# Performance work log

Measured on AMD Instinct MI355X. Metric: run time of the kernel, lower is better.

## Reference

```python
import jax, jax.numpy as jnp
import numpy as np

N = 50000
E = 800000
IN_DIM = 128
HIDDEN = 256
HP = HIDDEN // 3            # 85
HP2 = HIDDEN - 2 * HP       # 86
OUT_DIM = 40


def setup_inputs() -> dict:
    key = jax.random.key(0)
    ks = jax.random.split(key, 10)
    x = jax.random.normal(ks[0], (N, IN_DIM), dtype=jnp.float32)
    edge_index = jax.random.randint(ks[1], (2, E), 0, N, dtype=jnp.int64)
    s = 1.0 / np.sqrt(IN_DIM)
    W0 = jax.random.uniform(ks[2], (IN_DIM, HP), jnp.float32, -s, s)
    b0 = jax.random.uniform(ks[3], (HP,), jnp.float32, -s, s)
    W1 = jax.random.uniform(ks[4], (IN_DIM, HP), jnp.float32, -s, s)
    b1 = jax.random.uniform(ks[5], (HP,), jnp.float32, -s, s)
    W2 = jax.random.uniform(ks[6], (IN_DIM, HP2), jnp.float32, -s, s)
    b2 = jax.random.uniform(ks[7], (HP2,), jnp.float32, -s, s)
    sf = 1.0 / np.sqrt(HIDDEN)
    Wf = jax.random.uniform(ks[8], (HIDDEN, OUT_DIM), jnp.float32, -sf, sf)
    bf = jax.random.uniform(ks[9], (OUT_DIM,), jnp.float32, -sf, sf)
    return {"x": x, "edge_index": edge_index, "W0": W0, "b0": b0,
            "W1": W1, "b1": b1, "W2": W2, "b2": b2, "Wf": Wf, "bf": bf}


def _spmm(row, col, x, n):
    # adj @ x where adj[row[e], col[e]] = 1 : gather neighbor feats, scatter-add to row
    return jax.ops.segment_sum(x[col], row, num_segments=n)


def reference(x, edge_index, W0, b0, W1, b1, W2, b2, Wf, bf):
    n = x.shape[0]
    row, col = edge_index[0], edge_index[1]
    # out-degree of row nodes, clamped to min 1
    deg = jax.ops.segment_sum(jnp.ones((row.shape[0],), x.dtype), row, num_segments=n)
    deg_inv = 1.0 / jnp.maximum(deg, 1.0)
    # hop 0
    h0 = x @ W0 + b0
    # hop 1: (A x) * deg_inv
    ax = _spmm(row, col, x, n)
    h1 = (ax * deg_inv[:, None]) @ W1 + b1
    # hop 2: (A A x) * deg_inv^2
    aax = _spmm(row, col, ax, n)
    h2 = (aax * (deg_inv ** 2)[:, None]) @ W2 + b2
    h = jax.nn.relu(jnp.concatenate([h0, h1, h2], axis=1))
    # dropout inactive in eval mode
    return h @ Wf + bf
```

## Files before the change

kernel.cpp:

```cpp
#include <hip/hip_runtime.h>

#define N_NODES 50000
#define E_EDGES 800000
#define IN_DIM  128
#define OUT_DIM 40
#define NPAD    50176
#define NBKT    196
#define NBLK    256
#define EPB     3125

#define OFF_CNT   0
#define OFF_BASE  50176
#define OFF_DEG   100352
#define OFF_RS    150528
#define OFF_EPACK 200704
#define OFF_SCOL  1000704
#define OFF_WTBF  1800704
#define OFF_WF2T  1819136
#define OFF_BV    1826048
#define OFF_XBF   1826336
#define OFF_AXBF  (OFF_XBF  + NPAD * 64)
#define OFF_AAXBF (OFF_AXBF + NPAD * 64)
#define OFF_BTOT  (OFF_AAXBF + NPAD * 64)
#define OFF_BOFF  (OFF_BTOT + 256)

typedef short bf16x8 __attribute__((ext_vector_type(8)));
typedef float f32x4  __attribute__((ext_vector_type(4)));

__device__ __forceinline__ short f2bf(float f) {
    unsigned u = __float_as_uint(f);
    unsigned r = u + 0x7FFFu + ((u >> 16) & 1u);
    return (short)(r >> 16);
}

__device__ __forceinline__ bf16x8 cvt8(float4 a, float4 b) {
    bf16x8 v;
    v[0] = f2bf(a.x); v[1] = f2bf(a.y); v[2] = f2bf(a.z); v[3] = f2bf(a.w);
    v[4] = f2bf(b.x); v[5] = f2bf(b.y); v[6] = f2bf(b.z); v[7] = f2bf(b.w);
    return v;
}

__device__ __forceinline__ int block_excl_scan_256(int v, int* total_out,
                                                   int* wtot )
{
    const int t = threadIdx.x;
    const int lane = t & 63, wid = t >> 6;
    int sc = v;
    #pragma unroll
    for (int off = 1; off < 64; off <<= 1) {
        int tmp = __shfl_up(sc, off, 64);
        if (lane >= off) sc += tmp;
    }
    if (lane == 63) wtot[wid] = sc;
    __syncthreads();
    if (t == 0) {
        int a = 0;
        #pragma unroll
        for (int w2 = 0; w2 < 4; ++w2) { int tmp = wtot[w2]; wtot[w2] = a; a += tmp; }
        wtot[4] = a;
    }
    __syncthreads();
    *total_out = wtot[4];
    return sc - v + wtot[wid];
}

__global__ __launch_bounds__(256) void prep_kernel(
    const float* __restrict__ x, short* __restrict__ xbf,
    const int* __restrict__ row, int* __restrict__ cnt,
    const float* __restrict__ W0, const float* __restrict__ b0,
    const float* __restrict__ W1, const float* __restrict__ b1,
    const float* __restrict__ W2, const float* __restrict__ b2,
    const float* __restrict__ Wf,
    short* __restrict__ Wtbf, short* __restrict__ Wf2t,
    float* __restrict__ biasv)
{
    __shared__ int lbin[NBKT];
    const int t = threadIdx.x;
    const int b = blockIdx.x;

    if (b < 3136) {
        int idx = b * 256 + t;
        int node = idx >> 4;
        bf16x8 v;
        if (node < N_NODES) {
            const float4* rp = (const float4*)x + (size_t)idx * 2;
            v = cvt8(rp[0], rp[1]);
        } else {
            #pragma unroll
            for (int j = 0; j < 8; ++j) v[j] = 0;
        }
        *(bf16x8*)(xbf + (size_t)idx * 8) = v;
    } else if (b < 3136 + NBLK) {
        const int blk = b - 3136;
        if (t < NBKT) lbin[t] = 0;
        __syncthreads();
        const int e0 = blk * EPB;
        for (int i = t; i < EPB; i += 256)
            atomicAdd(&lbin[row[e0 + i] >> 8], 1);
        __syncthreads();
        if (t < NBKT) cnt[t * NBLK + blk] = lbin[t];
    } else {
        int idx = (b - 3392) * 256 + t;
        if (idx < 288 * 128) {
            int v = idx >> 7, k = idx & 127;
            int s = v / 96, local = v - 96 * s;
            float val = 0.0f;
            if (s == 0 && local < 85)      val = W0[k * 85 + local];
            else if (s == 1 && local < 85) val = W1[k * 85 + local];
            else if (s == 2 && local < 86) val = W2[k * 86 + local];
            Wtbf[idx] = f2bf(val);
        } else if (idx < 288 * 128 + 48 * 288) {
            int j2 = idx - 288 * 128;
            int c = j2 / 288, v = j2 - c * 288;
            int s = v / 96, local = v - 96 * s;
            float val = 0.0f;
            if (c < OUT_DIM && local < ((s == 2) ? 86 : 85))
                val = Wf[(s * 85 + local) * OUT_DIM + c];
            Wf2t[j2] = f2bf(val);
        } else if (idx < 288 * 128 + 48 * 288 + 288) {
            int v = idx - (288 * 128 + 48 * 288);
            int s = v / 96, local = v - 96 * s;
            float val = 0.0f;
            if (s == 0 && local < 85)      val = b0[local];
            else if (s == 1 && local < 85) val = b1[local];
            else if (s == 2 && local < 86) val = b2[local];
            biasv[v] = val;
        }
    }
}

__global__ __launch_bounds__(256) void scan_local_kernel(
    const int* __restrict__ cnt, int* __restrict__ base,
    int* __restrict__ btot)
{
    __shared__ int wtot[5];
    const int b = blockIdx.x;
    const int t = threadIdx.x;
    int v = cnt[b * NBLK + t];
    int total;
    int excl = block_excl_scan_256(v, &total, wtot);
    base[b * NBLK + t] = excl;
    if (t == 0) btot[b] = total;
}

__global__ __launch_bounds__(256) void scan_add_kernel(
    const int* __restrict__ btot, int* __restrict__ base)
{
    __shared__ int wtot[5];
    __shared__ int sh[256];
    const int t = threadIdx.x;
    const int b = blockIdx.x;
    int v = (t < NBKT) ? btot[t] : 0;
    int total;
    int excl = block_excl_scan_256(v, &total, wtot);
    sh[t] = excl;
    __syncthreads();
    int off = sh[b];
    base[b * NBLK + t] += off;
}

__global__ __launch_bounds__(256) void scatter_coarse_kernel(
    const int* __restrict__ row, const int* __restrict__ col,
    const int* __restrict__ base, unsigned int* __restrict__ epack)
{
    __shared__ int lcnt[NBKT];
    __shared__ int lbs[NBKT];
    const int t   = threadIdx.x;
    const int blk = blockIdx.x;
    if (t < NBKT) { lcnt[t] = 0; lbs[t] = base[t * NBLK + blk]; }
    __syncthreads();
    const int e0 = blk * EPB;
    for (int i = t; i < EPB; i += 256) {
        int r = row[e0 + i];
        int c = col[e0 + i];
        int cb = r >> 8;
        int loc = atomicAdd(&lcnt[cb], 1);
        epack[lbs[cb] + loc] = ((unsigned)(r & 255) << 16) | (unsigned)c;
    }
}

__global__ __launch_bounds__(256) void fine_sort_kernel(
    const unsigned int* __restrict__ epack,
    const int* __restrict__ base,
    int* __restrict__ sorted_col,
    int* __restrict__ deg, int* __restrict__ row_start)
{
    __shared__ int lhist[256];
    __shared__ int lbase[256];
    __shared__ int wtot[5];
    const int t  = threadIdx.x;
    const int cb = blockIdx.x;
    const int s  = base[cb * NBLK];
    const int e2 = (cb == NBKT - 1) ? E_EDGES : base[(cb + 1) * NBLK];

    lhist[t] = 0;
    __syncthreads();
    for (int i = s + t; i < e2; i += 256)
        atomicAdd(&lhist[epack[i] >> 16], 1);
    __syncthreads();

    int v = lhist[t];
    int total;
    int excl = block_excl_scan_256(v, &total, wtot);

    int node = cb * 256 + t;
    deg[node]       = v;
    row_start[node] = s + excl;
    lbase[t] = excl;
    __syncthreads();
    lhist[t] = 0;
    __syncthreads();

    for (int i = s + t; i < e2; i += 256) {
        unsigned p = epack[i];
        int rlo = p >> 16;
        int off = atomicAdd(&lhist[rlo], 1);
        sorted_col[s + lbase[rlo] + off] = (int)(p & 0xFFFFu);
    }
}

__global__ __launch_bounds__(256) void spmm_gather_kernel(
    const short* __restrict__ src,
    const int*   __restrict__ row_start,
    const int*   __restrict__ sorted_col,
    short*       __restrict__ dst)
{
    int node = (blockIdx.x * 256 + threadIdx.x) >> 4;
    int lane = threadIdx.x & 15;
    if (node >= N_NODES) return;
    int s = row_start[node];
    int e = row_start[node + 1];

    float acc[8];
    #pragma unroll
    for (int j = 0; j < 8; ++j) acc[j] = 0.0f;

    for (int i = s; i < e; i += 8) {
        const int nn = e - i;
        int cidx[8];
        #pragma unroll
        for (int j = 0; j < 8; ++j)
            cidx[j] = sorted_col[i + (j < nn ? j : 0)];
        uint4 v[8];
        #pragma unroll
        for (int j = 0; j < 8; ++j)
            v[j] = *(const uint4*)(src + (size_t)cidx[j] * IN_DIM + lane * 8);
        #pragma unroll
        for (int j = 0; j < 8; ++j) {
            if (j < nn) {
                acc[0] += __uint_as_float(v[j].x << 16);
                acc[1] += __uint_as_float(v[j].x & 0xFFFF0000u);
                acc[2] += __uint_as_float(v[j].y << 16);
                acc[3] += __uint_as_float(v[j].y & 0xFFFF0000u);
                acc[4] += __uint_as_float(v[j].z << 16);
                acc[5] += __uint_as_float(v[j].z & 0xFFFF0000u);
                acc[6] += __uint_as_float(v[j].w << 16);
                acc[7] += __uint_as_float(v[j].w & 0xFFFF0000u);
            }
        }
    }
    bf16x8 r;
    #pragma unroll
    for (int j = 0; j < 8; ++j) r[j] = f2bf(acc[j]);
    *(bf16x8*)(dst + (size_t)node * IN_DIM + lane * 8) = r;
}

#define HTS 296

__global__ __launch_bounds__(256) void dense_fused_kernel(
    const short* __restrict__ xbf,
    const short* __restrict__ axbf,
    const short* __restrict__ aaxbf,
    const int*   __restrict__ deg,
    const short* __restrict__ Wtbf,
    const short* __restrict__ Wf2t,
    const float* __restrict__ biasv,
    const float* __restrict__ bfin,
    float* __restrict__ out)
{
    __shared__ short wbuf[96 * 132];
    __shared__ short htile[64 * HTS];

    const int tid  = threadIdx.x;
    const int w    = tid >> 6;
    const int lane = tid & 63;
    const int il   = lane & 15;
    const int kq   = lane >> 4;
    const int m0   = blockIdx.x * 64 + w * 16;

    float dvj[4];
    #pragma unroll
    for (int j = 0; j < 4; ++j) {
        int node = m0 + kq * 4 + j;
        dvj[j] = 1.0f / fmaxf((float)deg[node], 1.0f);
    }

    #pragma unroll
    for (int s = 0; s < 3; ++s) {
        #pragma unroll
        for (int j = 0; j < 6; ++j) {
            int idx  = tid + j * 256;
            int brow = idx >> 4;
            int slot = idx & 15;
            uint4 v = *(const uint4*)(Wtbf + (size_t)(s * 96 + brow) * IN_DIM + slot * 8);
            *(uint4*)(wbuf + brow * 132 + slot * 8) = v;
        }
        __syncthreads();

        const short* __restrict__ src = (s == 0) ? xbf : (s == 1) ? axbf : aaxbf;
        const int arow = m0 + il;

        f32x4 acc[6];
        #pragma unroll
        for (int c = 0; c < 6; ++c)
            #pragma unroll
            for (int q = 0; q < 4; ++q) acc[c][q] = 0.0f;

        #pragma unroll
        for (int kk = 0; kk < 4; ++kk) {
            bf16x8 afrag = *(const bf16x8*)(
                src + (size_t)arow * IN_DIM + kk * 32 + kq * 8);
            #pragma unroll
            for (int c = 0; c < 6; ++c) {
                bf16x8 bfrag = *(const bf16x8*)(
                    wbuf + (c * 16 + il) * 132 + kk * 32 + kq * 8);
                acc[c] = __builtin_amdgcn_mfma_f32_16x16x32_bf16(
                    afrag, bfrag, acc[c], 0, 0, 0);
            }
        }

        #pragma unroll
        for (int j = 0; j < 4; ++j) {
            int nl = w * 16 + kq * 4 + j;
            float sc = (s == 0) ? 1.0f : (s == 1) ? dvj[j] : dvj[j] * dvj[j];
            #pragma unroll
            for (int c = 0; c < 6; ++c) {
                int vcol = s * 96 + c * 16 + il;
                float hv = fmaf(acc[c][j], sc, biasv[vcol]);
                htile[nl * HTS + vcol] = f2bf(fmaxf(hv, 0.0f));
            }
        }
        __syncthreads();
    }

    f32x4 acc2[3];
    #pragma unroll
    for (int cc = 0; cc < 3; ++cc)
        #pragma unroll
        for (int q = 0; q < 4; ++q) acc2[cc][q] = 0.0f;

    #pragma unroll
    for (int kk = 0; kk < 9; ++kk) {
        bf16x8 afrag = *(const bf16x8*)(
            htile + (w * 16 + il) * HTS + kk * 32 + kq * 8);
        #pragma unroll
        for (int cc = 0; cc < 3; ++cc) {
            bf16x8 bfrag = *(const bf16x8*)(
                Wf2t + (size_t)(cc * 16 + il) * 288 + kk * 32 + kq * 8);
            acc2[cc] = __builtin_amdgcn_mfma_f32_16x16x32_bf16(
                afrag, bfrag, acc2[cc], 0, 0, 0);
        }
    }

    #pragma unroll
    for (int cc = 0; cc < 3; ++cc) {
        int colo = cc * 16 + il;
        if (colo < OUT_DIM) {
            float b = bfin[colo];
            #pragma unroll
            for (int j = 0; j < 4; ++j) {
                int node = m0 + kq * 4 + j;
                if (node < N_NODES)
                    out[(size_t)node * OUT_DIM + colo] = acc2[cc][j] + b;
            }
        }
    }
}

extern "C" void kernel_launch(void* const* d_in, const int* in_sizes, int n_in,
                              void* d_out, int out_size, void* d_ws, size_t ws_size,
                              hipStream_t stream)
{
    const float* x  = (const float*)d_in[0];
    const int*   ei = (const int*)  d_in[1];
    const float* W0 = (const float*)d_in[2];
    const float* b0 = (const float*)d_in[3];
    const float* W1 = (const float*)d_in[4];
    const float* b1 = (const float*)d_in[5];
    const float* W2 = (const float*)d_in[6];
    const float* b2 = (const float*)d_in[7];
    const float* Wf = (const float*)d_in[8];
    const float* bf = (const float*)d_in[9];
    float* out = (float*)d_out;

    const int* row = ei;
    const int* col = ei + E_EDGES;

    int* wsw = (int*)d_ws;
    int*          cnt        = wsw + OFF_CNT;
    int*          base       = wsw + OFF_BASE;
    int*          deg        = wsw + OFF_DEG;
    int*          row_start  = wsw + OFF_RS;
    unsigned int* epack      = (unsigned int*)(wsw + OFF_EPACK);
    int*          sorted_col = wsw + OFF_SCOL;
    short*        Wtbf       = (short*)(wsw + OFF_WTBF);
    short*        Wf2t       = (short*)(wsw + OFF_WF2T);
    float*        biasv      = (float*)(wsw + OFF_BV);
    short*        xbf        = (short*)(wsw + OFF_XBF);
    short*        axbf       = (short*)(wsw + OFF_AXBF);
    short*        aaxbf      = (short*)(wsw + OFF_AAXBF);
    int*          btot       = wsw + OFF_BTOT;
    int*          boff       = wsw + OFF_BOFF;
    (void)boff; (void)ws_size; (void)in_sizes; (void)n_in; (void)out_size;

    dim3 blk(256);
    prep_kernel          <<<3136 + NBLK + 200, blk, 0, stream>>>(
        x, xbf, row, cnt, W0, b0, W1, b1, W2, b2, Wf, Wtbf, Wf2t, biasv);
    scan_local_kernel    <<<NBKT, blk, 0, stream>>>(cnt, base, btot);
    scan_add_kernel      <<<NBKT, blk, 0, stream>>>(btot, base);
    scatter_coarse_kernel<<<NBLK, blk, 0, stream>>>(row, col, base, epack);
    fine_sort_kernel     <<<NBKT, blk, 0, stream>>>(epack, base, sorted_col,
                                                    deg, row_start);

    const int sg = (N_NODES * 16 + 255) / 256;
    spmm_gather_kernel<<<sg, blk, 0, stream>>>(xbf,  row_start, sorted_col, axbf);
    spmm_gather_kernel<<<sg, blk, 0, stream>>>(axbf, row_start, sorted_col, aaxbf);

    dense_fused_kernel<<<NPAD / 64, blk, 0, stream>>>(
        xbf, axbf, aaxbf, deg, Wtbf, Wf2t, biasv, bf, out);
}
```

Before: 116.4 us.

## Fuse two-pass scan into one kernel and drop LDS weight staging in dense kernel

Replaces the local-scan plus add-offset pair with a single scan kernel where each block recomputes its global offset by summing all preceding counts, removing one launch and the btot round trip. The dense kernel no longer stages weights in shared memory. It reads B fragments straight from global (L1/L2-cached) memory, preloads all three A fragment sets up front, and gives each wave its own htile slice so the block-wide barriers go away. The cost is redundant reads of the count array (up to about 50K ints per block) and more global load traffic and register pressure in the dense kernel.

```diff
diff --git a/kernel.cpp b/kernel.cpp
--- a/kernel.cpp
+++ b/kernel.cpp
@@ -129,34 +129,30 @@
     }
 }
 
-__global__ __launch_bounds__(256) void scan_local_kernel(
-    const int* __restrict__ cnt, int* __restrict__ base,
-    int* __restrict__ btot)
+__global__ __launch_bounds__(256) void scan_fused_kernel(
+    const int* __restrict__ cnt, int* __restrict__ base)
 {
     __shared__ int wtot[5];
+    __shared__ int wsum[4];
     const int b = blockIdx.x;
     const int t = threadIdx.x;
+    const int lane = t & 63, wid = t >> 6;
+
     int v = cnt[b * NBLK + t];
     int total;
     int excl = block_excl_scan_256(v, &total, wtot);
-    base[b * NBLK + t] = excl;
-    if (t == 0) btot[b] = total;
-}
-
-__global__ __launch_bounds__(256) void scan_add_kernel(
-    const int* __restrict__ btot, int* __restrict__ base)
-{
-    __shared__ int wtot[5];
-    __shared__ int sh[256];
-    const int t = threadIdx.x;
-    const int b = blockIdx.x;
-    int v = (t < NBKT) ? btot[t] : 0;
-    int total;
-    int excl = block_excl_scan_256(v, &total, wtot);
-    sh[t] = excl;
-    __syncthreads();
-    int off = sh[b];
-    base[b * NBLK + t] += off;
+
+    int partial = 0;
+    const int lim = b * NBLK;
+    for (int i = t; i < lim; i += 256) partial += cnt[i];
+    #pragma unroll
+    for (int off = 32; off > 0; off >>= 1)
+        partial += __shfl_down(partial, off, 64);
+    if (lane == 0) wsum[wid] = partial;
+    __syncthreads();
+    int goff = wsum[0] + wsum[1] + wsum[2] + wsum[3];
+
+    base[b * NBLK + t] = excl + goff;
 }
 
 __global__ __launch_bounds__(256) void scatter_coarse_kernel(
@@ -278,8 +274,7 @@
     const float* __restrict__ bfin,
     float* __restrict__ out)
 {
-    __shared__ short wbuf[96 * 132];
-    __shared__ short htile[64 * HTS];
+    __shared__ short htile[4 * 16 * HTS];
 
     const int tid  = threadIdx.x;
     const int w    = tid >> 6;
@@ -287,7 +282,17 @@
     const int il   = lane & 15;
     const int kq   = lane >> 4;
     const int m0   = blockIdx.x * 64 + w * 16;
-
+    const int arow = m0 + il;
+
+    short* __restrict__ ht = htile + w * 16 * HTS;
+
+    bf16x8 afr[3][4];
+    #pragma unroll
+    for (int kk = 0; kk < 4; ++kk) {
+        afr[0][kk] = *(const bf16x8*)(xbf   + (size_t)arow * IN_DIM + kk * 32 + kq * 8);
+        afr[1][kk] = *(const bf16x8*)(axbf  + (size_t)arow * IN_DIM + kk * 32 + kq * 8);
+        afr[2][kk] = *(const bf16x8*)(aaxbf + (size_t)arow * IN_DIM + kk * 32 + kq * 8);
+    }
     float dvj[4];
     #pragma unroll
     for (int j = 0; j < 4; ++j) {
@@ -297,19 +302,6 @@
 
     #pragma unroll
     for (int s = 0; s < 3; ++s) {
-        #pragma unroll
-        for (int j = 0; j < 6; ++j) {
-            int idx  = tid + j * 256;
-            int brow = idx >> 4;
-            int slot = idx & 15;
-            uint4 v = *(const uint4*)(Wtbf + (size_t)(s * 96 + brow) * IN_DIM + slot * 8);
-            *(uint4*)(wbuf + brow * 132 + slot * 8) = v;
-        }
-        __syncthreads();
-
-        const short* __restrict__ src = (s == 0) ? xbf : (s == 1) ? axbf : aaxbf;
-        const int arow = m0 + il;
-
         f32x4 acc[6];
         #pragma unroll
         for (int c = 0; c < 6; ++c)
@@ -318,29 +310,26 @@
 
         #pragma unroll
         for (int kk = 0; kk < 4; ++kk) {
-            bf16x8 afrag = *(const bf16x8*)(
-                src + (size_t)arow * IN_DIM + kk * 32 + kq * 8);
             #pragma unroll
             for (int c = 0; c < 6; ++c) {
                 bf16x8 bfrag = *(const bf16x8*)(
-                    wbuf + (c * 16 + il) * 132 + kk * 32 + kq * 8);
+                    Wtbf + (size_t)(s * 96 + c * 16 + il) * IN_DIM + kk * 32 + kq * 8);
                 acc[c] = __builtin_amdgcn_mfma_f32_16x16x32_bf16(
-                    afrag, bfrag, acc[c], 0, 0, 0);
+                    afr[s][kk], bfrag, acc[c], 0, 0, 0);
             }
         }
 
         #pragma unroll
         for (int j = 0; j < 4; ++j) {
-            int nl = w * 16 + kq * 4 + j;
+            int nl = kq * 4 + j;
             float sc = (s == 0) ? 1.0f : (s == 1) ? dvj[j] : dvj[j] * dvj[j];
             #pragma unroll
             for (int c = 0; c < 6; ++c) {
                 int vcol = s * 96 + c * 16 + il;
                 float hv = fmaf(acc[c][j], sc, biasv[vcol]);
-                htile[nl * HTS + vcol] = f2bf(fmaxf(hv, 0.0f));
+                ht[nl * HTS + vcol] = f2bf(fmaxf(hv, 0.0f));
             }
         }
-        __syncthreads();
     }
 
     f32x4 acc2[3];
@@ -351,8 +340,7 @@
 
     #pragma unroll
     for (int kk = 0; kk < 9; ++kk) {
-        bf16x8 afrag = *(const bf16x8*)(
-            htile + (w * 16 + il) * HTS + kk * 32 + kq * 8);
+        bf16x8 afrag = *(const bf16x8*)(ht + il * HTS + kk * 32 + kq * 8);
         #pragma unroll
         for (int cc = 0; cc < 3; ++cc) {
             bf16x8 bfrag = *(const bf16x8*)(
@@ -409,15 +397,12 @@
     short*        xbf        = (short*)(wsw + OFF_XBF);
     short*        axbf       = (short*)(wsw + OFF_AXBF);
     short*        aaxbf      = (short*)(wsw + OFF_AAXBF);
-    int*          btot       = wsw + OFF_BTOT;
-    int*          boff       = wsw + OFF_BOFF;
-    (void)boff; (void)ws_size; (void)in_sizes; (void)n_in; (void)out_size;
+    (void)ws_size; (void)in_sizes; (void)n_in; (void)out_size;
 
     dim3 blk(256);
     prep_kernel          <<<3136 + NBLK + 200, blk, 0, stream>>>(
         x, xbf, row, cnt, W0, b0, W1, b1, W2, b2, Wf, Wtbf, Wf2t, biasv);
-    scan_local_kernel    <<<NBKT, blk, 0, stream>>>(cnt, base, btot);
-    scan_add_kernel      <<<NBKT, blk, 0, stream>>>(btot, base);
+    scan_fused_kernel    <<<NBKT, blk, 0, stream>>>(cnt, base);
     scatter_coarse_kernel<<<NBLK, blk, 0, stream>>>(row, col, base, epack);
     fine_sort_kernel     <<<NBKT, blk, 0, stream>>>(epack, base, sorted_col,
                                                     deg, row_start);
```

Result: slower. 162.5 us (+39.6%).
